# Optimization experiments

Measured on AMD Instinct MI355X. Metric: run time of the kernel, lower is better.

Reference implementation:

```python
import jax, jax.numpy as jnp
import numpy as np

USR_NUM = 100000
D_IN = 32
D_HID = 32
D_MID = 16
D_OUT = 2
N_EDGES = 1600000
EPS = 1e-16  # matches torch_geometric.utils.softmax denominator eps


def _glorot(key, shape):
    fan_in, fan_out = shape[0], shape[1]
    lim = np.sqrt(6.0 / (fan_in + fan_out))
    return jax.random.uniform(key, shape, jnp.float32, -lim, lim)


def setup_inputs() -> dict:
    key = jax.random.key(0)
    ks = jax.random.split(key, 16)
    inp = {
        "edge_index": jax.random.randint(ks[0], (2, N_EDGES), 0, USR_NUM, dtype=jnp.int64)
        if jax.config.jax_enable_x64 else jax.random.randint(ks[0], (2, N_EDGES), 0, USR_NUM).astype(jnp.int32),
        "emb": jax.random.normal(ks[1], (USR_NUM, D_IN), jnp.float32),
        # conv1: TransformerConv(32 -> 32, heads=1)
        "Wq1": _glorot(ks[2], (D_IN, D_HID)), "bq1": jnp.zeros((D_HID,), jnp.float32),
        "Wk1": _glorot(ks[3], (D_IN, D_HID)), "bk1": jnp.zeros((D_HID,), jnp.float32),
        "Wv1": _glorot(ks[4], (D_IN, D_HID)), "bv1": jnp.zeros((D_HID,), jnp.float32),
        "Ws1": _glorot(ks[5], (D_IN, D_HID)), "bs1": jnp.zeros((D_HID,), jnp.float32),
        # conv2: TransformerConv(32 -> 16, heads=1)
        "Wq2": _glorot(ks[6], (D_HID, D_MID)), "bq2": jnp.zeros((D_MID,), jnp.float32),
        "Wk2": _glorot(ks[7], (D_HID, D_MID)), "bk2": jnp.zeros((D_MID,), jnp.float32),
        "Wv2": _glorot(ks[8], (D_HID, D_MID)), "bv2": jnp.zeros((D_MID,), jnp.float32),
        "Ws2": _glorot(ks[9], (D_HID, D_MID)), "bs2": jnp.zeros((D_MID,), jnp.float32),
        # output: Linear(16 -> 2)
        "Wo": _glorot(ks[10], (D_MID, D_OUT)), "bo": jnp.zeros((D_OUT,), jnp.float32),
    }
    return inp


def transformer_conv(x, src, dst, Wq, bq, Wk, bk, Wv, bv, Ws, bs, n_nodes):
    # edge (j=src -> i=dst): alpha_ij = softmax_i( <q_i, k_j> / sqrt(d) )
    d = Wq.shape[1]
    q = (x @ Wq + bq)[dst]          # [E, d]
    k = (x @ Wk + bk)[src]          # [E, d]
    v = (x @ Wv + bv)[src]          # [E, d]
    alpha = jnp.sum(q * k, axis=-1) / jnp.sqrt(jnp.float32(d))  # [E]
    # segment softmax over incoming edges of each destination node
    seg_max = jax.ops.segment_max(alpha, dst, num_segments=n_nodes)  # [N]
    e = jnp.exp(alpha - seg_max[dst])
    seg_sum = jax.ops.segment_sum(e, dst, num_segments=n_nodes)      # [N]
    w = e / (seg_sum[dst] + EPS)
    agg = jax.ops.segment_sum(v * w[:, None], dst, num_segments=n_nodes)  # [N, d]
    return agg + x @ Ws + bs  # root/skip connection (PyG default root_weight=True)


def reference(edge_index, emb,
              Wq1, bq1, Wk1, bk1, Wv1, bv1, Ws1, bs1,
              Wq2, bq2, Wk2, bk2, Wv2, bv2, Ws2, bs2,
              Wo, bo):
    src, dst = edge_index[0], edge_index[1]
    h = transformer_conv(emb, src, dst, Wq1, bq1, Wk1, bk1, Wv1, bv1, Ws1, bs1, USR_NUM)
    h = jax.nn.relu(h)
    h = transformer_conv(h, src, dst, Wq2, bq2, Wk2, bk2, Wv2, bv2, Ws2, bs2, USR_NUM)
    h = jax.nn.relu(h)
    return h @ Wo + bo  # [N, 2]
```

## Files before the change

kernel.cpp:

```cpp
#include <hip/hip_runtime.h>
#include <hip/hip_bf16.h>

typedef __hip_bfloat16 bf16;
typedef unsigned int uint;
typedef unsigned short ushort;

#define N_NODES 100000
#define N_EDGES_C 1600000
#define NSB2 392
#define NSB2P 512
#define RND 2048
#define EPB (RND / 256)
#define NBIN 64
#define G_RAD ((N_EDGES_C + RND - 1) / RND)
#define HCAP 5632
#define NSLOT (NSB2 * 256)
#define NCHUNK 8
#define KEYN (256 * NCHUNK)

__device__ __forceinline__ float ldf(const void* p, long i, int isbf) {
    return isbf ? __bfloat162float(((const bf16*)p)[i]) : ((const float*)p)[i];
}
__device__ __forceinline__ int ldidx(const int* ei, long pos, int is64) {
    return is64 ? ei[2 * pos] : ei[pos];
}
__device__ __forceinline__ ushort bfb(float x) {
    bf16 h = __float2bfloat16(x);
    return *(ushort*)&h;
}
__device__ __forceinline__ float bl(uint u) { return __uint_as_float(u << 16); }
__device__ __forceinline__ float bh(uint u) { return __uint_as_float(u & 0xFFFF0000u); }

__global__ void setup_kernel(
    const void* emb, const int* ei,
    const void* Wq1, const void* bq1, const void* Wk1, const void* bk1,
    const void* Wv1, const void* bv1, const void* Ws1, const void* bs1,
    const void* Wq2, const void* bq2, const void* Wk2, const void* bk2,
    const void* Wv2, const void* bv2, const void* Ws2, const void* bs2,
    const void* Wo, const void* bo,
    int* flags, float* wp1, float* bp1, float* wp2, float* bp2, float* woF,
    int* curSB) {
    __shared__ int sf0;
    int t = threadIdx.x;
    if (t < 64) {
        const bf16* pb = (const bf16*)emb;
        int bad = 0;
        for (int i = t; i < 256; i += 64) {
            float v = __bfloat162float(pb[i]);
            if (!(v > -1.0e6f && v < 1.0e6f)) bad++;
        }
        int nz = 0;
        for (int i = 2 * t + 1; i < 256; i += 128) nz += (ei[i] != 0) ? 1 : 0;
#pragma unroll
        for (int m = 32; m >= 1; m >>= 1) {
            bad += __shfl_xor(bad, m, 64);
            nz  += __shfl_xor(nz, m, 64);
        }
        if (t == 0) {
            int f0 = (bad <= 8) ? 1 : 0;
            flags[0] = f0;
            flags[1] = (nz == 0) ? 1 : 0;
            sf0 = f0;
        }
    }
    __syncthreads();
    int isbf = sf0;
    for (int i = t; i < 1024; i += 256) {
        wp1[i]        = ldf(Wq1, i, isbf);
        wp1[1024 + i] = ldf(Wk1, i, isbf);
        wp1[2048 + i] = ldf(Wv1, i, isbf);
        wp1[3072 + i] = ldf(Ws1, i, isbf);
    }
    for (int i = t; i < 512; i += 256) {
        wp2[i]        = ldf(Wq2, i, isbf);
        wp2[512 + i]  = ldf(Wk2, i, isbf);
        wp2[1024 + i] = ldf(Wv2, i, isbf);
        wp2[1536 + i] = ldf(Ws2, i, isbf);
    }
    if (t < 32) {
        bp1[t] = ldf(bq1, t, isbf); bp1[32 + t] = ldf(bk1, t, isbf);
        bp1[64 + t] = ldf(bv1, t, isbf); bp1[96 + t] = ldf(bs1, t, isbf);
        woF[t] = ldf(Wo, t, isbf);
    }
    if (t < 16) {
        bp2[t] = ldf(bq2, t, isbf); bp2[16 + t] = ldf(bk2, t, isbf);
        bp2[32 + t] = ldf(bv2, t, isbf); bp2[48 + t] = ldf(bs2, t, isbf);
    }
    if (t < 2) woF[32 + t] = ldf(bo, t, isbf);
    curSB[t] = 0; curSB[t + 256] = 0;
}

template <int DOUT, bool RUNTIME_DTYPE>
__device__ __forceinline__ void node_linear_body(
    const void* __restrict__ X, const float* __restrict__ wpack,
    const float* __restrict__ bpack, const int* __restrict__ flags,
    float* __restrict__ q, ushort* __restrict__ kvb, float* __restrict__ s,
    int bid, float* __restrict__ sW, float* __restrict__ sbias, float* __restrict__ sX) {
    const int TPN = DOUT / 4;
    const int NPB = 256 / TPN;
    const int W_ELEMS = 4 * 32 * DOUT;

    const float4* wp4 = (const float4*)wpack;
    float4* sW4 = (float4*)sW;
    for (int i = threadIdx.x; i < W_ELEMS / 4; i += 256) sW4[i] = wp4[i];
    if (threadIdx.x < 4 * DOUT) sbias[threadIdx.x] = bpack[threadIdx.x];
    const int base = bid * NPB * 32;
    bool useBf = RUNTIME_DTYPE && (flags[0] != 0);
    if (useBf) {
        for (int i = threadIdx.x; i < NPB * 32; i += 256) {
            int g = base + i;
            float xv = (g < N_NODES * 32) ? __bfloat162float(((const bf16*)X)[g]) : 0.0f;
            sX[(i >> 5) * 36 + (i & 31)] = xv;
        }
    } else {
        for (int i = threadIdx.x; i < NPB * 32; i += 256) {
            int g = base + i;
            sX[(i >> 5) * 36 + (i & 31)] = (g < N_NODES * 32) ? ((const float*)X)[g] : 0.0f;
        }
    }
    __syncthreads();

    int l = threadIdx.x / TPN;
    int c4 = (threadIdx.x % TPN) * 4;
    int n = bid * NPB + l;
    if (n >= N_NODES) return;

    float xr[32];
#pragma unroll
    for (int j = 0; j < 8; j++) {
        float4 t4 = *(const float4*)&sX[l * 36 + 4 * j];
        xr[4 * j] = t4.x; xr[4 * j + 1] = t4.y; xr[4 * j + 2] = t4.z; xr[4 * j + 3] = t4.w;
    }
    float acc[4][4];
#pragma unroll
    for (int m = 0; m < 4; m++)
#pragma unroll
        for (int j = 0; j < 4; j++) acc[m][j] = sbias[m * DOUT + c4 + j];

#pragma unroll
    for (int t = 0; t < 32; t++) {
#pragma unroll
        for (int m = 0; m < 4; m++) {
            float4 w = *(const float4*)&sW[(m * 32 + t) * DOUT + c4];
            acc[m][0] += xr[t] * w.x;
            acc[m][1] += xr[t] * w.y;
            acc[m][2] += xr[t] * w.z;
            acc[m][3] += xr[t] * w.w;
        }
    }
    size_t o = (size_t)n * DOUT + c4;
    *(float4*)&q[o] = make_float4(acc[0][0], acc[0][1], acc[0][2], acc[0][3]);
    *(float4*)&s[o] = make_float4(acc[3][0], acc[3][1], acc[3][2], acc[3][3]);
    size_t okv = (size_t)n * 2 * DOUT + c4;
    ushort4 kp = make_ushort4(bfb(acc[1][0]), bfb(acc[1][1]), bfb(acc[1][2]), bfb(acc[1][3]));
    ushort4 vp = make_ushort4(bfb(acc[2][0]), bfb(acc[2][1]), bfb(acc[2][2]), bfb(acc[2][3]));
    *(ushort4*)&kvb[okv]        = kp;
    *(ushort4*)&kvb[okv + DOUT] = vp;
}

struct RadixS {
    int cnt[NSB2P]; int excl[NSB2P]; int gbase[NSB2P]; int wsum[4];
    uint sVal[RND]; ushort sSb[RND];
};
struct LinS { float sW[4096]; float sbias[128]; float sX[32 * 36]; };
union alignas(16) FusedS { RadixS r; LinS l; };

__global__ void __launch_bounds__(256, 4) fused_ra_nl(
    const int* __restrict__ ei, const int* __restrict__ flags,
    int* __restrict__ curSB, uint* __restrict__ pairsSB,
    const void* __restrict__ X, const float* __restrict__ wpack,
    const float* __restrict__ bpack,
    float* __restrict__ q, ushort* __restrict__ kvb, float* __restrict__ s) {
    __shared__ FusedS u;
    if (blockIdx.x >= G_RAD) {
        node_linear_body<32, true>(X, wpack, bpack, flags, q, kvb, s,
                                   (int)blockIdx.x - G_RAD, u.l.sW, u.l.sbias, u.l.sX);
        return;
    }
    int* cnt = u.r.cnt; int* excl = u.r.excl; int* gbase = u.r.gbase;
    uint* sVal = u.r.sVal; ushort* sSb = u.r.sSb;
    const int is64 = flags[1];
    int t = threadIdx.x;
    cnt[t] = 0; cnt[t + 256] = 0;
    __syncthreads();
    long base = (long)blockIdx.x * RND;

    int mySb[EPB]; int myRank[EPB]; uint myPk[EPB];
#pragma unroll
    for (int r = 0; r < EPB; r++) {
        long e = base + r * 256 + t;
        mySb[r] = -1;
        if (e < N_EDGES_C) {
            int d = ldidx(ei, (long)N_EDGES_C + e, is64);
            int src = ldidx(ei, e, is64);
            int sb = d >> 8;
            myPk[r] = (uint)src | ((uint)(d & 255) << 17);
            myRank[r] = atomicAdd(&cnt[sb], 1);
            mySb[r] = sb;
        }
    }
    __syncthreads();
    int v0 = cnt[2 * t], v1 = cnt[2 * t + 1];
    int sum2 = v0 + v1;
    int lane6 = t & 63, wid6 = t >> 6;
    int x = sum2;
#pragma unroll
    for (int off = 1; off < 64; off <<= 1) {
        int u2 = __shfl_up(x, off, 64);
        if (lane6 >= off) x += u2;
    }
    if (lane6 == 63) u.r.wsum[wid6] = x;
    __syncthreads();
    int wbase = 0;
#pragma unroll
    for (int w = 0; w < 4; w++) if (w < wid6) wbase += u.r.wsum[w];
    int basex = wbase + x - sum2;
    excl[2 * t]     = basex;
    excl[2 * t + 1] = basex + v0;
    __syncthreads();
#pragma unroll
    for (int r = 0; r < EPB; r++) {
        if (mySb[r] >= 0) {
            int pos = excl[mySb[r]] + myRank[r];
            sVal[pos] = myPk[r];
            sSb[pos] = (ushort)mySb[r];
        }
    }
    for (int i = t; i < NSB2P; i += 256)
        gbase[i] = (cnt[i] > 0) ? atomicAdd(&curSB[i], cnt[i]) : 0;
    __syncthreads();
    int tot = excl[NSB2P - 1] + cnt[NSB2P - 1];
    for (int i = t; i < tot; i += 256) {
        int sb = sSb[i];
        int gp = gbase[sb] + (i - excl[sb]);
        if (gp < HCAP)
            pairsSB[(size_t)sb * HCAP + gp] = sVal[i];
    }
}

__global__ void __launch_bounds__(512, 2) radix_b(
    const int* __restrict__ curSB, const uint* __restrict__ pairsSB,
    int* __restrict__ esrc,
    int* __restrict__ rowbeg, int* __restrict__ rowend,
    int* __restrict__ perm) {
    __shared__ uint sP[HCAP];
    __shared__ int dcnt[KEYN];
    __shared__ int dexcl[KEYN];
    __shared__ int wsum[4];
    __shared__ int hbin[NBIN], hbase[NBIN], hcur[NBIN];
    int sbh = blockIdx.x;
    int t = threadIdx.x;
    int n = min(curSB[sbh], HCAP);
    for (int i = t; i < KEYN; i += 512) dcnt[i] = 0;
    if (t < NBIN) { hbin[t] = 0; hcur[t] = 0; }
    if (t < 256) perm[sbh * 256 + t] = -1;
    __syncthreads();
    const uint* srcp = pairsSB + (size_t)sbh * HCAP;
    for (int i = t; i < n; i += 512) {
        uint pk = srcp[i];
        sP[i] = pk;
        int key = (int)((pk >> 17) & 255) * NCHUNK + (int)((pk & 0x1FFFFu) >> 14);
        atomicAdd(&dcnt[key], 1);
    }
    __syncthreads();
    int v = 0, myExcl = 0;
    if (t < 256) {
        const int kb = t * NCHUNK;
        int sum = 0;
#pragma unroll
        for (int j = 0; j < NCHUNK; j++) sum += dcnt[kb + j];
        v = sum;
        int lane6 = t & 63, wid6 = t >> 6;
        int x = v;
#pragma unroll
        for (int off = 1; off < 64; off <<= 1) {
            int u2 = __shfl_up(x, off, 64);
            if (lane6 >= off) x += u2;
        }
        if (lane6 == 63) wsum[wid6] = x;
        myExcl = x - v;
    }
    __syncthreads();
    if (t < 256) {
        int wid6 = t >> 6;
        int wbase = 0;
#pragma unroll
        for (int w = 0; w < 4; w++) if (w < wid6) wbase += wsum[w];
        myExcl += wbase;
        const int kb = t * NCHUNK;
        int run = myExcl;
#pragma unroll
        for (int j = 0; j < NCHUNK; j++) { dexcl[kb + j] = run; run += dcnt[kb + j]; }
    }
    __syncthreads();
    const int EB = sbh * HCAP;
    int dst = sbh * 256 + t;
    int mybin = -1;
    if (t < 256 && dst < N_NODES) {
        rowbeg[dst] = EB + min(myExcl, HCAP);
        rowend[dst] = EB + min(myExcl + v, HCAP);
        mybin = min(v, NBIN - 1);
        atomicAdd(&hbin[mybin], 1);
    }
    __syncthreads();
    if (t < 64) {
        int hv = hbin[t];
        int sfx = hv;
#pragma unroll
        for (int off = 1; off < 64; off <<= 1) {
            int u2 = __shfl_down(sfx, off, 64);
            if (t + off < 64) sfx += u2;
        }
        hbase[t] = sfx - hv;
    }
    __syncthreads();
    if (t < 256 && dst < N_NODES) {
        int r = atomicAdd(&hcur[mybin], 1);
        perm[sbh * 256 + hbase[mybin] + r] = dst;
    }
    for (int i = t; i < n; i += 512) {
        uint pk = sP[i];
        int key = (int)((pk >> 17) & 255) * NCHUNK + (int)((pk & 0x1FFFFu) >> 14);
        int p2 = atomicAdd(&dexcl[key], 1);
        if (p2 < HCAP) esrc[EB + p2] = (int)(pk & 0x1FFFF);
    }
}

template <int D, bool LAYER2>
__global__ void gather_attn(const int* __restrict__ perm,
                            const int* __restrict__ rowbeg, const int* __restrict__ rowend,
                            const int* __restrict__ esrc,
                            const float* __restrict__ q, const ushort* __restrict__ kvb,
                            const float* __restrict__ s,
                            const float* __restrict__ wp2,
                            const float* __restrict__ bp2,
                            const float* __restrict__ woF,
                            const int* __restrict__ flags,
                            float* __restrict__ q2o, ushort* __restrict__ kvb2o,
                            float* __restrict__ s2o,
                            void* __restrict__ out) {
    const int LPD = D / 8;
    const int G = 64 / LPD;
    __shared__ float sW2[LAYER2 ? 4 : 2048];
    __shared__ float sb2[LAYER2 ? 4 : 64];
    __shared__ float sH[LAYER2 ? 4 : 64 * 36];
    __shared__ int sDst[LAYER2 ? 4 : 64];

    if constexpr (!LAYER2) {
        for (int i = threadIdx.x; i < 2048; i += 256) sW2[i] = wp2[i];
        if (threadIdx.x < 64) sb2[threadIdx.x] = bp2[threadIdx.x];
    }

    int lane = threadIdx.x & 63;
    int wave = (blockIdx.x * blockDim.x + threadIdx.x) >> 6;
    int g = lane / LPD;
    int c = lane % LPD;
    int idx = wave * G + g;
    int dst = perm[idx];
    if constexpr (LAYER2) {
        if (dst < 0) return;
    }
    bool alive = (dst >= 0);

    const float rsq = (D == 32) ? 0.17677669529663689f : 0.25f;
    float4 qa = make_float4(0.f, 0.f, 0.f, 0.f), qb = qa;
    int beg = 0, end = 0;
    if (alive) {
        qa = *(const float4*)(q + (size_t)dst * D + 8 * c);
        qb = *(const float4*)(q + (size_t)dst * D + 8 * c + 4);
        beg = rowbeg[dst]; end = rowend[dst];
    }

    const char* kvbase = (const char*)kvb;
    const int ROW = 4 * D;
    const int koff = 16 * c;
    const int voff = 2 * D + 16 * c;

    float sum0 = 0.f, sum1 = 0.f;
    float a0[8] = {0,0,0,0,0,0,0,0};
    float a1[8] = {0,0,0,0,0,0,0,0};

    uint4 kq[4], vq[4];
#pragma unroll
    for (int r = 0; r < 4; r++) {
        int sn = (beg + r < end) ? esrc[beg + r] : 0;
        const char* p = kvbase + (size_t)sn * ROW;
        kq[r] = *(const uint4*)(p + koff);
        vq[r] = *(const uint4*)(p + voff);
    }

    for (int e = beg; e < end; e += 4) {
        uint4 kc[4], vc[4];
#pragma unroll
        for (int r = 0; r < 4; r++) { kc[r] = kq[r]; vc[r] = vq[r]; }
#pragma unroll
        for (int r = 0; r < 4; r++) {
            if (e + 4 + r < end) {
                const char* p = kvbase + (size_t)esrc[e + 4 + r] * ROW;
                kq[r] = *(const uint4*)(p + koff);
                vq[r] = *(const uint4*)(p + voff);
            }
        }
#pragma unroll
        for (int r = 0; r < 4; r++) {
            if (e + r < end) {
                uint4 kA = kc[r], vA = vc[r];
                float pd = qa.x * bl(kA.x) + qa.y * bh(kA.x) + qa.z * bl(kA.y) + qa.w * bh(kA.y)
                         + qb.x * bl(kA.z) + qb.y * bh(kA.z) + qb.z * bl(kA.w) + qb.w * bh(kA.w);
#pragma unroll
                for (int m = LPD / 2; m >= 1; m >>= 1) pd += __shfl_xor(pd, m, LPD);
                float ex = __expf(fminf(fmaxf(pd * rsq, -80.0f), 80.0f));
                if (r & 1) {
                    sum1 += ex;
                    a1[0] += bl(vA.x) * ex; a1[1] += bh(vA.x) * ex;
                    a1[2] += bl(vA.y) * ex; a1[3] += bh(vA.y) * ex;
                    a1[4] += bl(vA.z) * ex; a1[5] += bh(vA.z) * ex;
                    a1[6] += bl(vA.w) * ex; a1[7] += bh(vA.w) * ex;
                } else {
                    sum0 += ex;
                    a0[0] += bl(vA.x) * ex; a0[1] += bh(vA.x) * ex;
                    a0[2] += bl(vA.y) * ex; a0[3] += bh(vA.y) * ex;
                    a0[4] += bl(vA.z) * ex; a0[5] += bh(vA.z) * ex;
                    a0[6] += bl(vA.w) * ex; a0[7] += bh(vA.w) * ex;
                }
            }
        }
    }
    float inv = 1.0f / (sum0 + sum1 + 1e-16f);
    float4 sa = make_float4(0.f, 0.f, 0.f, 0.f), sbv = sa;
    if (alive) {
        sa  = *(const float4*)(s + (size_t)dst * D + 8 * c);
        sbv = *(const float4*)(s + (size_t)dst * D + 8 * c + 4);
    }
    float h[8];
    h[0] = (a0[0] + a1[0]) * inv + sa.x;  h[1] = (a0[1] + a1[1]) * inv + sa.y;
    h[2] = (a0[2] + a1[2]) * inv + sa.z;  h[3] = (a0[3] + a1[3]) * inv + sa.w;
    h[4] = (a0[4] + a1[4]) * inv + sbv.x; h[5] = (a0[5] + a1[5]) * inv + sbv.y;
    h[6] = (a0[6] + a1[6]) * inv + sbv.z; h[7] = (a0[7] + a1[7]) * inv + sbv.w;
#pragma unroll
    for (int j = 0; j < 8; j++) h[j] = h[j] > 0.0f ? h[j] : 0.0f;

    if constexpr (!LAYER2) {
        int gl = (threadIdx.x >> 6) * G + g;
        if (alive) {
            *(float4*)&sH[gl * 36 + 8 * c]     = make_float4(h[0], h[1], h[2], h[3]);
            *(float4*)&sH[gl * 36 + 8 * c + 4] = make_float4(h[4], h[5], h[6], h[7]);
        }
        if (c == 0) sDst[gl] = dst;
        __syncthreads();
        int l = threadIdx.x >> 2;
        int c4 = (threadIdx.x & 3) * 4;
        int nd = sDst[l];
        if (nd >= 0) {
            float acc2[4][4];
#pragma unroll
            for (int m = 0; m < 4; m++)
#pragma unroll
                for (int j = 0; j < 4; j++) acc2[m][j] = sb2[m * 16 + c4 + j];
#pragma unroll
            for (int t2 = 0; t2 < 32; t2++) {
                float xv = sH[l * 36 + t2];
#pragma unroll
                for (int m = 0; m < 4; m++) {
                    float4 w = *(const float4*)&sW2[(m * 32 + t2) * 16 + c4];
                    acc2[m][0] += xv * w.x;
                    acc2[m][1] += xv * w.y;
                    acc2[m][2] += xv * w.z;
                    acc2[m][3] += xv * w.w;
                }
            }
            size_t o = (size_t)nd * 16 + c4;
            *(float4*)&q2o[o] = make_float4(acc2[0][0], acc2[0][1], acc2[0][2], acc2[0][3]);
            *(float4*)&s2o[o] = make_float4(acc2[3][0], acc2[3][1], acc2[3][2], acc2[3][3]);
            size_t okv = (size_t)nd * 32 + c4;
            ushort4 kp = make_ushort4(bfb(acc2[1][0]), bfb(acc2[1][1]), bfb(acc2[1][2]), bfb(acc2[1][3]));
            ushort4 vp = make_ushort4(bfb(acc2[2][0]), bfb(acc2[2][1]), bfb(acc2[2][2]), bfb(acc2[2][3]));
            *(ushort4*)&kvb2o[okv]      = kp;
            *(ushort4*)&kvb2o[okv + 16] = vp;
        }
    } else {
        float p0 = 0.f, p1 = 0.f;
#pragma unroll
        for (int j = 0; j < 8; j++) {
            p0 += h[j] * woF[(8 * c + j) * 2 + 0];
            p1 += h[j] * woF[(8 * c + j) * 2 + 1];
        }
#pragma unroll
        for (int m = LPD / 2; m >= 1; m >>= 1) {
            p0 += __shfl_xor(p0, m, LPD);
            p1 += __shfl_xor(p1, m, LPD);
        }
        if (c == 0) {
            float o0 = p0 + woF[32];
            float o1 = p1 + woF[33];
            if (flags[0]) {
                ((bf16*)out)[dst * 2 + 0] = __float2bfloat16(o0);
                ((bf16*)out)[dst * 2 + 1] = __float2bfloat16(o1);
            } else {
                ((float*)out)[dst * 2 + 0] = o0;
                ((float*)out)[dst * 2 + 1] = o1;
            }
        }
    }
}

extern "C" void kernel_launch(void* const* d_in, const int* in_sizes, int n_in,
                              void* d_out, int out_size, void* d_ws, size_t ws_size,
                              hipStream_t stream) {
    const int* ei  = (const int*)d_in[0];
    const void* emb = d_in[1];
    const void *Wq1 = d_in[2],  *bq1 = d_in[3];
    const void *Wk1 = d_in[4],  *bk1 = d_in[5];
    const void *Wv1 = d_in[6],  *bv1 = d_in[7];
    const void *Ws1 = d_in[8],  *bs1 = d_in[9];
    const void *Wq2 = d_in[10], *bq2 = d_in[11];
    const void *Wk2 = d_in[12], *bk2 = d_in[13];
    const void *Wv2 = d_in[14], *bv2 = d_in[15];
    const void *Ws2 = d_in[16], *bs2 = d_in[17];
    const void *Wo  = d_in[18], *bo  = d_in[19];

    const size_t ND   = (size_t)N_NODES * 32;
    const size_t ND16 = (size_t)N_NODES * 16;
    const size_t SBTOT = (size_t)NSB2 * HCAP;
    float* base   = (float*)d_ws;
    int*   flags  = (int*)base;
    float* wp1    = base + 64;
    float* bp1    = wp1 + 4096;
    float* wp2    = bp1 + 128;
    float* bp2    = wp2 + 2048;
    float* woF    = bp2 + 64;
    int*   curSB  = (int*)(woF + 64);
    int*   rowbeg = curSB + 512;
    int*   rowend = rowbeg + N_NODES;
    int*   perm   = rowend + N_NODES;
    float* p      = (float*)(perm + NSLOT);
    p = (float*)(((uintptr_t)p + 127) & ~(uintptr_t)127);
    float* q      = p; p += ND;
    float* s      = p; p += ND;
    ushort* kvb   = (ushort*)p; p += ND;
    float* q2     = p; p += ND16;
    float* s2     = p; p += ND16;
    ushort* kvb2  = (ushort*)p; p += ND16;
    int*   esrc   = (int*)p; p += SBTOT;
    uint*  pairsSB = (uint*)p;

    const int B = 256;
    const int gNL32  = (N_NODES + 31) / 32;
    const int gFused = G_RAD + gNL32;
    const int gG1    = NSLOT / 64;
    const int gG2    = NSLOT / 128;

    setup_kernel<<<1, B, 0, stream>>>(emb, ei,
        Wq1, bq1, Wk1, bk1, Wv1, bv1, Ws1, bs1,
        Wq2, bq2, Wk2, bk2, Wv2, bv2, Ws2, bs2, Wo, bo,
        flags, wp1, bp1, wp2, bp2, woF, curSB);

    fused_ra_nl<<<gFused, B, 0, stream>>>(ei, flags, curSB, pairsSB,
                                          emb, wp1, bp1, q, kvb, s);

    radix_b<<<NSB2, 512, 0, stream>>>(curSB, pairsSB, esrc, rowbeg, rowend, perm);

    gather_attn<32, false><<<gG1, B, 0, stream>>>(
        perm, rowbeg, rowend, esrc, q, kvb, s, wp2, bp2, nullptr, flags,
        q2, kvb2, s2, nullptr);

    gather_attn<16, true><<<gG2, B, 0, stream>>>(
        perm, rowbeg, rowend, esrc, q2, kvb2, s2, nullptr, nullptr, woF, flags,
        nullptr, nullptr, nullptr, d_out);
}
```

Measured before the change: 259.3 us.

## Specialize layer-2 gather: split K and V lanes with per-node 4-lane groups

The templated gather kernel is split into two dedicated kernels. The layer-2 kernel now gives each destination node a group of 4 lanes, where 2 lanes compute the q·k dot product and 2 lanes accumulate the weighted V, instead of 2 lanes doing both. The edge-source loads are prefetched 4 edges ahead, and the grid is sized to match 16 nodes per wave. This is meant to raise parallelism and memory-level parallelism on the sparse layer-2 gather, at the cost of more lanes and threads per node plus extra shuffles per edge.

```diff
diff --git a/kernel.cpp b/kernel.cpp
--- a/kernel.cpp
+++ b/kernel.cpp
@@ -326,30 +326,25 @@
     }
 }
 
-template <int D, bool LAYER2>
-__global__ void gather_attn(const int* __restrict__ perm,
-                            const int* __restrict__ rowbeg, const int* __restrict__ rowend,
-                            const int* __restrict__ esrc,
-                            const float* __restrict__ q, const ushort* __restrict__ kvb,
-                            const float* __restrict__ s,
-                            const float* __restrict__ wp2,
-                            const float* __restrict__ bp2,
-                            const float* __restrict__ woF,
-                            const int* __restrict__ flags,
-                            float* __restrict__ q2o, ushort* __restrict__ kvb2o,
-                            float* __restrict__ s2o,
-                            void* __restrict__ out) {
-    const int LPD = D / 8;
-    const int G = 64 / LPD;
-    __shared__ float sW2[LAYER2 ? 4 : 2048];
-    __shared__ float sb2[LAYER2 ? 4 : 64];
-    __shared__ float sH[LAYER2 ? 4 : 64 * 36];
-    __shared__ int sDst[LAYER2 ? 4 : 64];
-
-    if constexpr (!LAYER2) {
-        for (int i = threadIdx.x; i < 2048; i += 256) sW2[i] = wp2[i];
-        if (threadIdx.x < 64) sb2[threadIdx.x] = bp2[threadIdx.x];
-    }
+__global__ void gather_attn_l1(const int* __restrict__ perm,
+                               const int* __restrict__ rowbeg, const int* __restrict__ rowend,
+                               const int* __restrict__ esrc,
+                               const float* __restrict__ q, const ushort* __restrict__ kvb,
+                               const float* __restrict__ s,
+                               const float* __restrict__ wp2,
+                               const float* __restrict__ bp2,
+                               float* __restrict__ q2o, ushort* __restrict__ kvb2o,
+                               float* __restrict__ s2o) {
+    const int D = 32;
+    const int LPD = 4;
+    const int G = 16;
+    __shared__ float sW2[2048];
+    __shared__ float sb2[64];
+    __shared__ float sH[64 * 36];
+    __shared__ int sDst[64];
+
+    for (int i = threadIdx.x; i < 2048; i += 256) sW2[i] = wp2[i];
+    if (threadIdx.x < 64) sb2[threadIdx.x] = bp2[threadIdx.x];
 
     int lane = threadIdx.x & 63;
     int wave = (blockIdx.x * blockDim.x + threadIdx.x) >> 6;
@@ -357,12 +352,9 @@
     int c = lane % LPD;
     int idx = wave * G + g;
     int dst = perm[idx];
-    if constexpr (LAYER2) {
-        if (dst < 0) return;
-    }
     bool alive = (dst >= 0);
 
-    const float rsq = (D == 32) ? 0.17677669529663689f : 0.25f;
+    const float rsq = 0.17677669529663689f;
     float4 qa = make_float4(0.f, 0.f, 0.f, 0.f), qb = qa;
     int beg = 0, end = 0;
     if (alive) {
@@ -440,66 +432,161 @@
 #pragma unroll
     for (int j = 0; j < 8; j++) h[j] = h[j] > 0.0f ? h[j] : 0.0f;
 
-    if constexpr (!LAYER2) {
-        int gl = (threadIdx.x >> 6) * G + g;
-        if (alive) {
-            *(float4*)&sH[gl * 36 + 8 * c]     = make_float4(h[0], h[1], h[2], h[3]);
-            *(float4*)&sH[gl * 36 + 8 * c + 4] = make_float4(h[4], h[5], h[6], h[7]);
-        }
-        if (c == 0) sDst[gl] = dst;
-        __syncthreads();
-        int l = threadIdx.x >> 2;
-        int c4 = (threadIdx.x & 3) * 4;
-        int nd = sDst[l];
-        if (nd >= 0) {
-            float acc2[4][4];
-#pragma unroll
-            for (int m = 0; m < 4; m++)
-#pragma unroll
-                for (int j = 0; j < 4; j++) acc2[m][j] = sb2[m * 16 + c4 + j];
-#pragma unroll
-            for (int t2 = 0; t2 < 32; t2++) {
-                float xv = sH[l * 36 + t2];
-#pragma unroll
-                for (int m = 0; m < 4; m++) {
-                    float4 w = *(const float4*)&sW2[(m * 32 + t2) * 16 + c4];
-                    acc2[m][0] += xv * w.x;
-                    acc2[m][1] += xv * w.y;
-                    acc2[m][2] += xv * w.z;
-                    acc2[m][3] += xv * w.w;
+    int gl = (threadIdx.x >> 6) * G + g;
+    if (alive) {
+        *(float4*)&sH[gl * 36 + 8 * c]     = make_float4(h[0], h[1], h[2], h[3]);
+        *(float4*)&sH[gl * 36 + 8 * c + 4] = make_float4(h[4], h[5], h[6], h[7]);
+    }
+    if (c == 0) sDst[gl] = dst;
+    __syncthreads();
+    int l = threadIdx.x >> 2;
+    int c4 = (threadIdx.x & 3) * 4;
+    int nd = sDst[l];
+    if (nd >= 0) {
+        float acc2[4][4];
+#pragma unroll
+        for (int m = 0; m < 4; m++)
+#pragma unroll
+            for (int j = 0; j < 4; j++) acc2[m][j] = sb2[m * 16 + c4 + j];
+#pragma unroll
+        for (int t2 = 0; t2 < 32; t2++) {
+            float xv = sH[l * 36 + t2];
+#pragma unroll
+            for (int m = 0; m < 4; m++) {
+                float4 w = *(const float4*)&sW2[(m * 32 + t2) * 16 + c4];
+                acc2[m][0] += xv * w.x;
+                acc2[m][1] += xv * w.y;
+                acc2[m][2] += xv * w.z;
+                acc2[m][3] += xv * w.w;
+            }
+        }
+        size_t o = (size_t)nd * 16 + c4;
+        *(float4*)&q2o[o] = make_float4(acc2[0][0], acc2[0][1], acc2[0][2], acc2[0][3]);
+        *(float4*)&s2o[o] = make_float4(acc2[3][0], acc2[3][1], acc2[3][2], acc2[3][3]);
+        size_t okv = (size_t)nd * 32 + c4;
+        ushort4 kp = make_ushort4(bfb(acc2[1][0]), bfb(acc2[1][1]), bfb(acc2[1][2]), bfb(acc2[1][3]));
+        ushort4 vp = make_ushort4(bfb(acc2[2][0]), bfb(acc2[2][1]), bfb(acc2[2][2]), bfb(acc2[2][3]));
+        *(ushort4*)&kvb2o[okv]      = kp;
+        *(ushort4*)&kvb2o[okv + 16] = vp;
+    }
+}
+
+__global__ void gather_attn_l2(const int* __restrict__ perm,
+                               const int* __restrict__ rowbeg, const int* __restrict__ rowend,
+                               const int* __restrict__ esrc,
+                               const float* __restrict__ q, const ushort* __restrict__ kvb,
+                               const float* __restrict__ s,
+                               const float* __restrict__ woF,
+                               const int* __restrict__ flags,
+                               void* __restrict__ out) {
+    const int D = 16;
+    const int LG = 4;
+    const int KL = 2;
+    const int G  = 16;
+
+    int lane = threadIdx.x & 63;
+    int W = (blockIdx.x * blockDim.x + threadIdx.x) >> 6;
+    int g = lane / LG;
+    int sub = lane % LG;
+    bool isK = (sub < KL);
+    int cv = sub - KL;
+    int idx = W * G + g;
+    int dst = perm[idx];
+    if (dst < 0) return;
+
+    const float rsq = 0.25f;
+    float qacc[8] = {0,0,0,0,0,0,0,0};
+    if (isK) {
+        float4 qa = *(const float4*)(q + (size_t)dst * D + 8 * sub);
+        float4 qb = *(const float4*)(q + (size_t)dst * D + 8 * sub + 4);
+        qacc[0] = qa.x; qacc[1] = qa.y; qacc[2] = qa.z; qacc[3] = qa.w;
+        qacc[4] = qb.x; qacc[5] = qb.y; qacc[6] = qb.z; qacc[7] = qb.w;
+    }
+    int beg = rowbeg[dst], end = rowend[dst];
+
+    const char* kvbase = (const char*)kvb + 16 * sub;
+    const int ROW = 4 * D;
+
+    float sum = 0.f;
+
+    uint4 rv[4];
+    int sn1[4];
+#pragma unroll
+    for (int r = 0; r < 4; r++) {
+        int sn = (beg + r < end) ? esrc[beg + r] : 0;
+        rv[r] = *(const uint4*)(kvbase + (size_t)sn * ROW);
+    }
+#pragma unroll
+    for (int r = 0; r < 4; r++)
+        sn1[r] = (beg + 4 + r < end) ? esrc[beg + 4 + r] : 0;
+
+    for (int e = beg; e < end; e += 4) {
+        uint4 rc[4];
+#pragma unroll
+        for (int r = 0; r < 4; r++) rc[r] = rv[r];
+#pragma unroll
+        for (int r = 0; r < 4; r++) {
+            if (e + 4 + r < end)
+                rv[r] = *(const uint4*)(kvbase + (size_t)sn1[r] * ROW);
+        }
+#pragma unroll
+        for (int r = 0; r < 4; r++) {
+            if (e + 8 + r < end) sn1[r] = esrc[e + 8 + r];
+        }
+#pragma unroll
+        for (int r = 0; r < 4; r++) {
+            if (e + r < end) {
+                uint4 rA = rc[r];
+                float pd = 0.f;
+                if (isK) {
+                    pd = qacc[0] * bl(rA.x) + qacc[1] * bh(rA.x)
+                       + qacc[2] * bl(rA.y) + qacc[3] * bh(rA.y)
+                       + qacc[4] * bl(rA.z) + qacc[5] * bh(rA.z)
+                       + qacc[6] * bl(rA.w) + qacc[7] * bh(rA.w);
+                }
+                pd += __shfl_xor(pd, 1, KL);
+                float pdx = __shfl_xor(pd, KL, LG);
+                float pdf = isK ? pd : pdx;
+                float ex = __expf(fminf(fmaxf(pdf * rsq, -80.0f), 80.0f));
+                sum += ex;
+                if (!isK) {
+                    qacc[0] += bl(rA.x) * ex; qacc[1] += bh(rA.x) * ex;
+                    qacc[2] += bl(rA.y) * ex; qacc[3] += bh(rA.y) * ex;
+                    qacc[4] += bl(rA.z) * ex; qacc[5] += bh(rA.z) * ex;
+                    qacc[6] += bl(rA.w) * ex; qacc[7] += bh(rA.w) * ex;
                 }
             }
-            size_t o = (size_t)nd * 16 + c4;
-            *(float4*)&q2o[o] = make_float4(acc2[0][0], acc2[0][1], acc2[0][2], acc2[0][3]);
-            *(float4*)&s2o[o] = make_float4(acc2[3][0], acc2[3][1], acc2[3][2], acc2[3][3]);
-            size_t okv = (size_t)nd * 32 + c4;
-            ushort4 kp = make_ushort4(bfb(acc2[1][0]), bfb(acc2[1][1]), bfb(acc2[1][2]), bfb(acc2[1][3]));
-            ushort4 vp = make_ushort4(bfb(acc2[2][0]), bfb(acc2[2][1]), bfb(acc2[2][2]), bfb(acc2[2][3]));
-            *(ushort4*)&kvb2o[okv]      = kp;
-            *(ushort4*)&kvb2o[okv + 16] = vp;
-        }
-    } else {
-        float p0 = 0.f, p1 = 0.f;
+        }
+    }
+    float inv = 1.0f / (sum + 1e-16f);
+    float p0 = 0.f, p1 = 0.f;
+    if (!isK) {
+        float4 sa  = *(const float4*)(s + (size_t)dst * D + 8 * cv);
+        float4 sbv = *(const float4*)(s + (size_t)dst * D + 8 * cv + 4);
+        float h[8];
+        h[0] = qacc[0] * inv + sa.x;  h[1] = qacc[1] * inv + sa.y;
+        h[2] = qacc[2] * inv + sa.z;  h[3] = qacc[3] * inv + sa.w;
+        h[4] = qacc[4] * inv + sbv.x; h[5] = qacc[5] * inv + sbv.y;
+        h[6] = qacc[6] * inv + sbv.z; h[7] = qacc[7] * inv + sbv.w;
+#pragma unroll
+        for (int j = 0; j < 8; j++) h[j] = h[j] > 0.0f ? h[j] : 0.0f;
 #pragma unroll
         for (int j = 0; j < 8; j++) {
-            p0 += h[j] * woF[(8 * c + j) * 2 + 0];
-            p1 += h[j] * woF[(8 * c + j) * 2 + 1];
-        }
-#pragma unroll
-        for (int m = LPD / 2; m >= 1; m >>= 1) {
-            p0 += __shfl_xor(p0, m, LPD);
-            p1 += __shfl_xor(p1, m, LPD);
-        }
-        if (c == 0) {
-            float o0 = p0 + woF[32];
-            float o1 = p1 + woF[33];
-            if (flags[0]) {
-                ((bf16*)out)[dst * 2 + 0] = __float2bfloat16(o0);
-                ((bf16*)out)[dst * 2 + 1] = __float2bfloat16(o1);
-            } else {
-                ((float*)out)[dst * 2 + 0] = o0;
-                ((float*)out)[dst * 2 + 1] = o1;
-            }
+            p0 += h[j] * woF[(8 * cv + j) * 2 + 0];
+            p1 += h[j] * woF[(8 * cv + j) * 2 + 1];
+        }
+    }
+    p0 += __shfl_xor(p0, 1, 2);
+    p1 += __shfl_xor(p1, 1, 2);
+    if (sub == KL) {
+        float o0 = p0 + woF[32];
+        float o1 = p1 + woF[33];
+        if (flags[0]) {
+            ((bf16*)out)[dst * 2 + 0] = __float2bfloat16(o0);
+            ((bf16*)out)[dst * 2 + 1] = __float2bfloat16(o1);
+        } else {
+            ((float*)out)[dst * 2 + 0] = o0;
+            ((float*)out)[dst * 2 + 1] = o1;
         }
     }
 }
@@ -548,7 +635,7 @@
     const int gNL32  = (N_NODES + 31) / 32;
     const int gFused = G_RAD + gNL32;
     const int gG1    = NSLOT / 64;
-    const int gG2    = NSLOT / 128;
+    const int gG2    = NSLOT * 4 / 256;
 
     setup_kernel<<<1, B, 0, stream>>>(emb, ei,
         Wq1, bq1, Wk1, bk1, Wv1, bv1, Ws1, bs1,
@@ -560,11 +647,9 @@
 
     radix_b<<<NSB2, 512, 0, stream>>>(curSB, pairsSB, esrc, rowbeg, rowend, perm);
 
-    gather_attn<32, false><<<gG1, B, 0, stream>>>(
-        perm, rowbeg, rowend, esrc, q, kvb, s, wp2, bp2, nullptr, flags,
-        q2, kvb2, s2, nullptr);
-
-    gather_attn<16, true><<<gG2, B, 0, stream>>>(
-        perm, rowbeg, rowend, esrc, q2, kvb2, s2, nullptr, nullptr, woF, flags,
-        nullptr, nullptr, nullptr, d_out);
-}
+    gather_attn_l1<<<gG1, B, 0, stream>>>(
+        perm, rowbeg, rowend, esrc, q, kvb, s, wp2, bp2, q2, kvb2, s2);
+
+    gather_attn_l2<<<gG2, B, 0, stream>>>(
+        perm, rowbeg, rowend, esrc, q2, kvb2, s2, woF, flags, d_out);
+}
```

New measurement: 259.6 us. About the same (+0.1%).
